# Optimization experiments

Measured on AMD Instinct MI355X. Metric: run time of the kernel, lower is better.

## Reference

```python
import jax, jax.numpy as jnp
import numpy as np

D_MODEL = 1024
N_HEADS = 16
HEAD_DIM = D_MODEL // N_HEADS
SCALE = HEAD_DIM ** -0.5
MIN_VAL = jnp.finfo(jnp.float32).min


def setup_inputs() -> dict:
    key = jax.random.key(0)
    ks = jax.random.split(key, 7)
    B, T = 1, 2048
    s = D_MODEL ** -0.5
    return {
        "x": jax.random.normal(ks[0], (B, T, D_MODEL), dtype=jnp.float32),
        "Wq": jax.random.normal(ks[1], (D_MODEL, D_MODEL), dtype=jnp.float32) * s,
        "Wk1": jax.random.normal(ks[2], (D_MODEL, D_MODEL), dtype=jnp.float32) * s,
        "Wk2": jax.random.normal(ks[3], (D_MODEL, D_MODEL), dtype=jnp.float32) * s,
        "Wv": jax.random.normal(ks[4], (D_MODEL, D_MODEL), dtype=jnp.float32) * s,
        "Wo": jax.random.normal(ks[5], (D_MODEL, D_MODEL), dtype=jnp.float32) * s,
        "lambda_logit": jnp.zeros((N_HEADS,), dtype=jnp.float32),  # logit(0.5)=0
    }


def _split_heads(y):
    B, T, _ = y.shape
    return y.reshape(B, T, N_HEADS, HEAD_DIM).transpose(0, 2, 1, 3)  # [B,H,T,hd]


def reference(x, Wq, Wk1, Wk2, Wv, Wo, lambda_logit):
    B, T, _ = x.shape
    q = _split_heads(x @ Wq.T)
    k1 = _split_heads(x @ Wk1.T)
    k2 = _split_heads(x @ Wk2.T)
    v = _split_heads(x @ Wv.T)

    s1 = jnp.einsum("bhqd,bhkd->bhqk", q, k1) * SCALE
    s2 = jnp.einsum("bhqd,bhkd->bhqk", q, k2) * SCALE

    causal = jnp.arange(T)[None, :] <= jnp.arange(T)[:, None]  # [T,T] keep mask
    s1 = jnp.where(causal[None, None], s1, MIN_VAL)
    s2 = jnp.where(causal[None, None], s2, MIN_VAL)

    attn_exp = jax.nn.softmax(s1, axis=-1)
    attn_noise = jax.nn.softmax(s2, axis=-1)
    lam = jax.nn.sigmoid(lambda_logit)[None, :, None, None]
    attn = attn_exp - lam * attn_noise
    denom = jnp.maximum(jnp.sum(jnp.abs(attn), axis=-1, keepdims=True), 1e-6)
    attn = attn / denom

    out = jnp.einsum("bhqk,bhkd->bhqd", attn, v)
    out = out.transpose(0, 2, 1, 3).reshape(B, T, D_MODEL)
    return out @ Wo.T
```

## Files before the change

kernel.cpp:

```cpp
#include <hip/hip_runtime.h>

#define T_SEQ 2048
#define DM 1024
#define NH 16
#define HD 64
#define SC2 0.1803368801111731f
#define LS 72

typedef unsigned short u16;
typedef unsigned int u32;
typedef __attribute__((ext_vector_type(8))) short bf16x8;
typedef __attribute__((ext_vector_type(4))) float f32x4;

static __device__ __forceinline__ f32x4 mfma16(bf16x8 a, bf16x8 b, f32x4 c) {
    return __builtin_amdgcn_mfma_f32_16x16x32_bf16(a, b, c, 0, 0, 0);
}
static __device__ __forceinline__ float bf2f(u16 u) {
    union { u32 i; float f; } v; v.i = ((u32)u) << 16; return v.f;
}
static __device__ __forceinline__ u16 f2bf(float f) {
    union { float f; u32 i; } v; v.f = f;
    u32 x = v.i;
    x += 0x7FFFu + ((x >> 16) & 1u);
    return (u16)(x >> 16);
}
static __device__ __forceinline__ u16 f2bf_t(float f) {
    union { float f; u32 i; } v; v.f = f;
    return (u16)(v.i >> 16);
}
static __device__ __forceinline__ u32 pk2(float lo, float hi) {
    return (u32)f2bf(lo) | ((u32)f2bf(hi) << 16);
}
static __device__ __forceinline__ float qsum16(float v) {
#pragma unroll
    for (int o = 1; o < 16; o <<= 1) v += __shfl_xor(v, o, 64);
    return v;
}
static __device__ __forceinline__ float ex2(float x) {
    return __builtin_amdgcn_exp2f(x);
}

static __device__ __forceinline__ void gl16(const u16* g, u16* l) {
    __builtin_amdgcn_global_load_lds(
        (const __attribute__((address_space(1))) void*)g,
        (__attribute__((address_space(3))) void*)l,
        16, 0, 0);
}

template <int NISS>
static __device__ __forceinline__ void stage_async(const u16* src, size_t row0,
                                                   size_t lds_, size_t col0,
                                                   u16* dst, int tid) {
#pragma unroll
    for (int it = 0; it < NISS; it++) {
        int r = it * 32 + (tid >> 3);
        int cg = (tid & 7) ^ (r & 7);
        gl16(&src[(row0 + r) * lds_ + col0 + cg * 8], &dst[(it * 256 + tid) * 8]);
    }
}
static __device__ __forceinline__ bf16x8 frag(const u16* buf, int R, int co) {
    return *(const bf16x8*)(&buf[R * 64 + co]);
}

__global__ __launch_bounds__(256) void detect_dtype(const u16* __restrict__ x,
                                                    int* __restrict__ flag) {
    __shared__ int tot;
    const int tid = threadIdx.x;
    if (tid == 0) tot = 0;
    __syncthreads();
    int c = 0;
#pragma unroll
    for (int i = 0; i < 4; i++) {
        u16 v = x[2 * (tid * 4 + i)];
        int e = (v >> 7) & 0xFF;
        c += (e >= 110 && e <= 140) ? 1 : 0;
    }
    atomicAdd(&tot, c);
    __syncthreads();
    if (tid == 0) *flag = (tot >= 512) ? 1 : 0;
}

__global__ __launch_bounds__(256) void cvt_bf16(
    const int* __restrict__ flag,
    const float* __restrict__ x, const float* __restrict__ wq,
    const float* __restrict__ wk1, const float* __restrict__ wk2,
    const float* __restrict__ wv, const float* __restrict__ wo,
    u16* __restrict__ xc, u16* __restrict__ wqc, u16* __restrict__ wk1c,
    u16* __restrict__ wk2c, u16* __restrict__ wvc, u16* __restrict__ woc) {
    if (*flag) return;
    const int b = blockIdx.x;
    const int tid = threadIdx.x;
    const float* src;
    u16* dst;
    int rel;
    if (b < 1024)      { src = x;   dst = xc;   rel = b; }
    else if (b < 1536) { src = wq;  dst = wqc;  rel = b - 1024; }
    else if (b < 2048) { src = wk1; dst = wk1c; rel = b - 1536; }
    else if (b < 2560) { src = wk2; dst = wk2c; rel = b - 2048; }
    else if (b < 3072) { src = wv;  dst = wvc;  rel = b - 2560; }
    else               { src = wo;  dst = woc;  rel = b - 3072; }
    size_t idx = (size_t)rel * 2048 + (size_t)tid * 8;
    const float* s = src + idx;
    uint4 a = *(const uint4*)s;
    uint4 bq = *(const uint4*)(s + 4);
    const float* af = (const float*)&a;
    const float* bf = (const float*)&bq;
    uint4 r;
    r.x = pk2(af[0], af[1]); r.y = pk2(af[2], af[3]);
    r.z = pk2(bf[0], bf[1]); r.w = pk2(bf[2], bf[3]);
    *(uint4*)(dst + idx) = r;
}

__global__ __launch_bounds__(256) void qkv_gemm(
    const int* __restrict__ flag,
    const void* __restrict__ x0, const void* __restrict__ wq0,
    const void* __restrict__ wk10, const void* __restrict__ wk20,
    const void* __restrict__ wv0,
    const u16* __restrict__ xc, const u16* __restrict__ wqc,
    const u16* __restrict__ wk1c, const u16* __restrict__ wk2c,
    const u16* __restrict__ wvc,
    u16* __restrict__ qd, u16* __restrict__ k1d, u16* __restrict__ k2d,
    u16* __restrict__ vtd) {
    __shared__ __align__(16) u16 As[2][128 * 64];
    __shared__ __align__(16) u16 Bs[2][128 * 64];

    const int f = *flag;
    const int tid = threadIdx.x;
    const int w = blockIdx.x >> 3;
    const int n0 = (blockIdx.x & 7) * 128;
    const int m0 = blockIdx.y * 128;
    const u16* xb = f ? (const u16*)x0 : xc;
    const u16* Bb;
    if (w == 0)      Bb = f ? (const u16*)wq0  : wqc;
    else if (w == 1) Bb = f ? (const u16*)wk10 : wk1c;
    else if (w == 2) Bb = f ? (const u16*)wk20 : wk2c;
    else             Bb = f ? (const u16*)wv0  : wvc;

    const int lane = tid & 63, wave = tid >> 6;
    const int lr = lane & 15, quad = lane >> 4;
    const int wm = (wave >> 1) * 64, wn = (wave & 1) * 64;
    const int sw = lr & 7;

    f32x4 acc[4][4];
#pragma unroll
    for (int i = 0; i < 4; i++)
#pragma unroll
        for (int j = 0; j < 4; j++) acc[i][j] = (f32x4){0.f, 0.f, 0.f, 0.f};

    stage_async<4>(xb, m0, DM, 0, As[0], tid);
    stage_async<4>(Bb, n0, DM, 0, Bs[0], tid);
    for (int k0 = 0; k0 < DM; k0 += 64) {
        const int cur = (k0 >> 6) & 1;
        __syncthreads();
        if (k0 + 64 < DM) {
            stage_async<4>(xb, m0, DM, k0 + 64, As[cur ^ 1], tid);
            stage_async<4>(Bb, n0, DM, k0 + 64, Bs[cur ^ 1], tid);
        }
#pragma unroll
        for (int kk = 0; kk < 2; kk++) {
            const int co = ((kk * 4 + quad) ^ sw) * 8;
            bf16x8 af[4], bfr[4];
#pragma unroll
            for (int i = 0; i < 4; i++) af[i] = frag(As[cur], wm + i * 16 + lr, co);
#pragma unroll
            for (int j = 0; j < 4; j++) bfr[j] = frag(Bs[cur], wn + j * 16 + lr, co);
#pragma unroll
            for (int i = 0; i < 4; i++)
#pragma unroll
                for (int j = 0; j < 4; j++) acc[i][j] = mfma16(af[i], bfr[j], acc[i][j]);
        }
    }

#pragma unroll
    for (int i = 0; i < 4; i++)
#pragma unroll
        for (int j = 0; j < 4; j++)
#pragma unroll
            for (int r = 0; r < 4; r++) {
                int t = m0 + wm + i * 16 + quad * 4 + r;
                int o = n0 + wn + j * 16 + lr;
                float val = acc[i][j][r];
                if (w == 0) val *= SC2;
                u16 vbits = f2bf(val);
                int hh = o >> 6, d0 = o & 63;
                if (w == 3)
                    vtd[((size_t)hh * HD + d0) * T_SEQ + t] = vbits;
                else
                    ((w == 0) ? qd : (w == 1) ? k1d : k2d)[((size_t)hh * T_SEQ + t) * HD + d0] = vbits;
            }
}

#define ATTN_MAP()                                            \
    const int b = blockIdx.x;                                 \
    const int par = b >> 9;                                   \
    const int rem = b & 511;                                  \
    const int h = rem & 15;                                   \
    const int bi = rem >> 4;                                  \
    const int qt = (bi < 16) ? bi : 47 - bi;                  \
    const int t0 = qt * 64;                                   \
    const int tid = threadIdx.x;                              \
    const int lane = tid & 63, wave = tid >> 6;               \
    const int lr = lane & 15, quad = lane >> 4;               \
    const int wm = wave * 16;                                 \
    const int sw = lr & 7;

__global__ __launch_bounds__(256) void attn_a(
    const u16* __restrict__ qg, const u16* __restrict__ k1g,
    const u16* __restrict__ k2g, float* __restrict__ zp) {
    __shared__ __align__(16) u16 k1s[64 * 64];
    __shared__ __align__(16) u16 k2s[64 * 64];
    ATTN_MAP();

    const u16* qh = qg + (size_t)h * T_SEQ * HD;
    const u16* k1h = k1g + (size_t)h * T_SEQ * HD;
    const u16* k2h = k2g + (size_t)h * T_SEQ * HD;

    bf16x8 aq[2];
#pragma unroll
    for (int kk = 0; kk < 2; kk++)
        aq[kk] = *(const bf16x8*)(&qh[(size_t)(t0 + wm + lr) * HD + kk * 32 + quad * 8]);

    float z1a[4] = {0.f, 0.f, 0.f, 0.f}, z2a[4] = {0.f, 0.f, 0.f, 0.f};

    for (int kt = par; kt <= qt; kt += 4) {
        __syncthreads();
        stage_async<2>(k1h, (size_t)kt * 64, HD, 0, k1s, tid);
        stage_async<2>(k2h, (size_t)kt * 64, HD, 0, k2s, tid);
        __syncthreads();

        f32x4 sa[4], sb[4];
#pragma unroll
        for (int j = 0; j < 4; j++) { sa[j] = (f32x4){0.f,0.f,0.f,0.f}; sb[j] = (f32x4){0.f,0.f,0.f,0.f}; }
#pragma unroll
        for (int kk = 0; kk < 2; kk++) {
            const int co = ((kk * 4 + quad) ^ sw) * 8;
#pragma unroll
            for (int j = 0; j < 4; j++) {
                sa[j] = mfma16(aq[kk], frag(k1s, j * 16 + lr, co), sa[j]);
                sb[j] = mfma16(aq[kk], frag(k2s, j * 16 + lr, co), sb[j]);
            }
        }

        if (kt < qt) {
#pragma unroll
            for (int r = 0; r < 4; r++)
#pragma unroll
                for (int j = 0; j < 4; j++) {
                    z1a[r] += ex2(sa[j][r]);
                    z2a[r] += ex2(sb[j][r]);
                }
        } else {
#pragma unroll
            for (int r = 0; r < 4; r++) {
                const int grow = t0 + wm + quad * 4 + r;
#pragma unroll
                for (int j = 0; j < 4; j++) {
                    int gcol = kt * 64 + j * 16 + lr;
                    if (gcol <= grow) {
                        z1a[r] += ex2(sa[j][r]);
                        z2a[r] += ex2(sb[j][r]);
                    }
                }
            }
        }
    }

#pragma unroll
    for (int r = 0; r < 4; r++) {
        float s1 = qsum16(z1a[r]);
        float s2 = qsum16(z2a[r]);
        if (lr == 0) {
            int row = t0 + wm + quad * 4 + r;
            zp[((size_t)(par * 2 + 0) * NH + h) * T_SEQ + row] = s1;
            zp[((size_t)(par * 2 + 1) * NH + h) * T_SEQ + row] = s2;
        }
    }
}

__global__ __launch_bounds__(256) void attn_b(
    const u16* __restrict__ qg, const u16* __restrict__ k1g,
    const u16* __restrict__ k2g, const u16* __restrict__ vtg,
    const float* __restrict__ zp, const void* __restrict__ lamsrc,
    const int* __restrict__ flag,
    float* __restrict__ dpart, u16* __restrict__ opart) {
    __shared__ __align__(16) u16 k1s[64 * 64];
    __shared__ __align__(16) u16 k2s[64 * 64];
    __shared__ __align__(16) u16 vs[64 * 64];
    __shared__ __align__(16) u16 ps[4][16 * LS];
    ATTN_MAP();

    const int f = *flag;
    float lamlogit = f ? bf2f(((const u16*)lamsrc)[h]) : ((const float*)lamsrc)[h];
    const float lam = 1.0f / (1.0f + __expf(-lamlogit));

    const u16* qh = qg + (size_t)h * T_SEQ * HD;
    const u16* k1h = k1g + (size_t)h * T_SEQ * HD;
    const u16* k2h = k2g + (size_t)h * T_SEQ * HD;
    const u16* vh = vtg + (size_t)h * HD * T_SEQ;

    bf16x8 aq[2];
#pragma unroll
    for (int kk = 0; kk < 2; kk++)
        aq[kk] = *(const bf16x8*)(&qh[(size_t)(t0 + wm + lr) * HD + kk * 32 + quad * 8]);

    float z1l[4], z2l[4];
#pragma unroll
    for (int r = 0; r < 4; r++) {
        int row = t0 + wm + quad * 4 + r;
        float z1 = 0.f, z2 = 0.f;
#pragma unroll
        for (int p = 0; p < 4; p++) {
            z1 += zp[((size_t)(p * 2 + 0) * NH + h) * T_SEQ + row];
            z2 += zp[((size_t)(p * 2 + 1) * NH + h) * T_SEQ + row];
        }
        z1l[r] = -__log2f(z1);
        z2l[r] = __log2f(lam) - __log2f(z2);
    }

    f32x4 oac[4];
#pragma unroll
    for (int j = 0; j < 4; j++) oac[j] = (f32x4){0.f, 0.f, 0.f, 0.f};
    float dacc[4] = {0.f, 0.f, 0.f, 0.f};

    for (int kt = par; kt <= qt; kt += 2) {
        __syncthreads();
        stage_async<2>(k1h, (size_t)kt * 64, HD, 0, k1s, tid);
        stage_async<2>(k2h, (size_t)kt * 64, HD, 0, k2s, tid);
        stage_async<2>(vh, 0, T_SEQ, (size_t)kt * 64, vs, tid);
        __syncthreads();

        f32x4 sa[4], sb[4];
#pragma unroll
        for (int j = 0; j < 4; j++) { sa[j] = (f32x4){0.f,0.f,0.f,0.f}; sb[j] = (f32x4){0.f,0.f,0.f,0.f}; }
#pragma unroll
        for (int kk = 0; kk < 2; kk++) {
            const int co = ((kk * 4 + quad) ^ sw) * 8;
#pragma unroll
            for (int j = 0; j < 4; j++) {
                sa[j] = mfma16(aq[kk], frag(k1s, j * 16 + lr, co), sa[j]);
                sb[j] = mfma16(aq[kk], frag(k2s, j * 16 + lr, co), sb[j]);
            }
        }

        if (kt < qt) {
#pragma unroll
            for (int r = 0; r < 4; r++)
#pragma unroll
                for (int j = 0; j < 4; j++) {
                    float p = ex2(sa[j][r] + z1l[r]) - ex2(sb[j][r] + z2l[r]);
                    dacc[r] += fabsf(p);
                    ps[wave][(quad * 4 + r) * LS + j * 16 + lr] = f2bf_t(p);
                }
        } else {
#pragma unroll
            for (int r = 0; r < 4; r++) {
                const int grow = t0 + wm + quad * 4 + r;
#pragma unroll
                for (int j = 0; j < 4; j++) {
                    int gcol = kt * 64 + j * 16 + lr;
                    float p = 0.f;
                    if (gcol <= grow)
                        p = ex2(sa[j][r] + z1l[r]) - ex2(sb[j][r] + z2l[r]);
                    dacc[r] += fabsf(p);
                    ps[wave][(quad * 4 + r) * LS + j * 16 + lr] = f2bf_t(p);
                }
            }
        }

#pragma unroll
        for (int kk = 0; kk < 2; kk++) {
            bf16x8 pa = *(const bf16x8*)(&ps[wave][lr * LS + kk * 32 + quad * 8]);
            const int co = ((kk * 4 + quad) ^ sw) * 8;
#pragma unroll
            for (int j = 0; j < 4; j++)
                oac[j] = mfma16(pa, frag(vs, j * 16 + lr, co), oac[j]);
        }
    }

#pragma unroll
    for (int r = 0; r < 4; r++) {
        float ds = qsum16(dacc[r]);
        if (lr == 0) {
            int row = t0 + wm + quad * 4 + r;
            dpart[((size_t)par * NH + h) * T_SEQ + row] = ds;
        }
    }
#pragma unroll
    for (int j = 0; j < 4; j++)
#pragma unroll
        for (int r = 0; r < 4; r++) {
            int row = t0 + wm + quad * 4 + r;
            opart[(size_t)par * T_SEQ * DM + (size_t)row * DM + h * HD + j * 16 + lr] =
                f2bf(oac[j][r]);
        }
}

__global__ __launch_bounds__(256) void normalize_o(
    const u16* __restrict__ opart, const float* __restrict__ dpart,
    u16* __restrict__ ao) {
    int g = blockIdx.x * 256 + threadIdx.x;
    int t = g >> 7;
    int cc = g & 127;
    int d0 = cc * 8;
    int h = d0 >> 6;
    float dsum = dpart[(size_t)h * T_SEQ + t] + dpart[(size_t)(NH + h) * T_SEQ + t];
    float rs = 1.f / fmaxf(dsum, 1e-6f);
    uint4 a = *(const uint4*)(&opart[(size_t)t * DM + d0]);
    uint4 bqq = *(const uint4*)(&opart[(size_t)T_SEQ * DM + (size_t)t * DM + d0]);
    const u32* au = (const u32*)&a;
    const u32* bu = (const u32*)&bqq;
    uint4 out;
    u32* ou = (u32*)&out;
#pragma unroll
    for (int i = 0; i < 4; i++) {
        float lo = (bf2f((u16)(au[i] & 0xFFFF)) + bf2f((u16)(bu[i] & 0xFFFF))) * rs;
        float hi = (bf2f((u16)(au[i] >> 16)) + bf2f((u16)(bu[i] >> 16))) * rs;
        ou[i] = pk2(lo, hi);
    }
    *(uint4*)(&ao[(size_t)t * DM + d0]) = out;
}

__global__ __launch_bounds__(256) void out_gemm(
    const u16* __restrict__ ab, const void* __restrict__ wo0,
    const u16* __restrict__ woc, const int* __restrict__ flag,
    void* __restrict__ outp) {
    __shared__ __align__(16) u16 As[2][64 * 64];
    __shared__ __align__(16) u16 Bs[2][64 * 64];

    const int f = *flag;
    const u16* wb = f ? (const u16*)wo0 : woc;
    const int n0 = blockIdx.x * 64;
    const int m0 = blockIdx.y * 64;
    const int tid = threadIdx.x;
    const int lane = tid & 63, wave = tid >> 6;
    const int lr = lane & 15, quad = lane >> 4;
    const int wm = (wave >> 1) * 32, wn = (wave & 1) * 32;
    const int sw = lr & 7;

    f32x4 acc[2][2];
#pragma unroll
    for (int i = 0; i < 2; i++)
#pragma unroll
        for (int j = 0; j < 2; j++) acc[i][j] = (f32x4){0.f, 0.f, 0.f, 0.f};

    stage_async<2>(ab, m0, DM, 0, As[0], tid);
    stage_async<2>(wb, n0, DM, 0, Bs[0], tid);
    for (int k0 = 0; k0 < DM; k0 += 64) {
        const int cur = (k0 >> 6) & 1;
        __syncthreads();
        if (k0 + 64 < DM) {
            stage_async<2>(ab, m0, DM, k0 + 64, As[cur ^ 1], tid);
            stage_async<2>(wb, n0, DM, k0 + 64, Bs[cur ^ 1], tid);
        }
#pragma unroll
        for (int kk = 0; kk < 2; kk++) {
            const int co = ((kk * 4 + quad) ^ sw) * 8;
            bf16x8 af[2], bfr[2];
#pragma unroll
            for (int i = 0; i < 2; i++) af[i] = frag(As[cur], wm + i * 16 + lr, co);
#pragma unroll
            for (int j = 0; j < 2; j++) bfr[j] = frag(Bs[cur], wn + j * 16 + lr, co);
#pragma unroll
            for (int i = 0; i < 2; i++)
#pragma unroll
                for (int j = 0; j < 2; j++) acc[i][j] = mfma16(af[i], bfr[j], acc[i][j]);
        }
    }

#pragma unroll
    for (int i = 0; i < 2; i++)
#pragma unroll
        for (int j = 0; j < 2; j++)
#pragma unroll
            for (int r = 0; r < 4; r++) {
                int t = m0 + wm + i * 16 + quad * 4 + r;
                int o = n0 + wn + j * 16 + lr;
                float val = acc[i][j][r];
                if (f)
                    ((u16*)outp)[(size_t)t * DM + o] = f2bf(val);
                else
                    ((float*)outp)[(size_t)t * DM + o] = val;
            }
}

extern "C" void kernel_launch(void* const* d_in, const int* in_sizes, int n_in,
                              void* d_out, int out_size, void* d_ws, size_t ws_size,
                              hipStream_t stream) {
    char* ws = (char*)d_ws;
    int* flag = (int*)(ws + 0);
    float* zp    = (float*)(ws + ((size_t)1 << 20));
    float* dpart = (float*)(ws + ((size_t)2 << 20));
    u16* qd  = (u16*)(ws + ((size_t)16 << 20));
    u16* k1d = (u16*)(ws + ((size_t)20 << 20));
    u16* k2d = (u16*)(ws + ((size_t)24 << 20));
    u16* vtd = (u16*)(ws + ((size_t)28 << 20));
    u16* ao  = (u16*)(ws + ((size_t)32 << 20));
    u16* opart = (u16*)(ws + ((size_t)36 << 20));
    u16* xc   = (u16*)(ws + ((size_t)44 << 20));
    u16* wqc  = (u16*)(ws + ((size_t)48 << 20));
    u16* wk1c = (u16*)(ws + ((size_t)50 << 20));
    u16* wk2c = (u16*)(ws + ((size_t)52 << 20));
    u16* wvc  = (u16*)(ws + ((size_t)54 << 20));
    u16* woc  = (u16*)(ws + ((size_t)56 << 20));

    detect_dtype<<<dim3(1), 256, 0, stream>>>((const u16*)d_in[0], flag);
    cvt_bf16<<<dim3(3584), 256, 0, stream>>>(
        flag, (const float*)d_in[0], (const float*)d_in[1], (const float*)d_in[2],
        (const float*)d_in[3], (const float*)d_in[4], (const float*)d_in[5],
        xc, wqc, wk1c, wk2c, wvc, woc);
    qkv_gemm<<<dim3(32, 16), 256, 0, stream>>>(
        flag, d_in[0], d_in[1], d_in[2], d_in[3], d_in[4],
        xc, wqc, wk1c, wk2c, wvc, qd, k1d, k2d, vtd);
    attn_a<<<dim3(2048), 256, 0, stream>>>(qd, k1d, k2d, zp);
    attn_b<<<dim3(1024), 256, 0, stream>>>(qd, k1d, k2d, vtd, zp, d_in[6], flag,
                                           dpart, opart);
    normalize_o<<<dim3(1024), 256, 0, stream>>>(opart, dpart, ao);
    out_gemm<<<dim3(16, 32), 256, 0, stream>>>(ao, d_in[5], woc, flag, d_out);
}
```

Baseline: 192.5 us.

## Process two 64-row query groups per attention block to reuse staged K/V tiles

Both attention kernels now handle a 128-row query tile per block, split into two 64-row groups that share each staged K1/K2/V tile in shared memory. This halves the block count and the global-to-LDS staging traffic per unit of work, which is meant to cut memory and synchronisation overhead. It costs more registers (doubled accumulators and Q fragments) and gives fewer blocks, which may reduce occupancy and load balance across CUs.

```diff
diff --git a/kernel.cpp b/kernel.cpp
--- a/kernel.cpp
+++ b/kernel.cpp
@@ -190,75 +190,86 @@
             }
 }
 
-#define ATTN_MAP()                                            \
-    const int b = blockIdx.x;                                 \
-    const int par = b >> 9;                                   \
-    const int rem = b & 511;                                  \
-    const int h = rem & 15;                                   \
-    const int bi = rem >> 4;                                  \
-    const int qt = (bi < 16) ? bi : 47 - bi;                  \
-    const int t0 = qt * 64;                                   \
-    const int tid = threadIdx.x;                              \
-    const int lane = tid & 63, wave = tid >> 6;               \
-    const int lr = lane & 15, quad = lane >> 4;               \
-    const int wm = wave * 16;                                 \
-    const int sw = lr & 7;
-
 __global__ __launch_bounds__(256) void attn_a(
     const u16* __restrict__ qg, const u16* __restrict__ k1g,
     const u16* __restrict__ k2g, float* __restrict__ zp) {
     __shared__ __align__(16) u16 k1s[64 * 64];
     __shared__ __align__(16) u16 k2s[64 * 64];
-    ATTN_MAP();
+    const int b = blockIdx.x;
+    const int par = b >> 8;
+    const int rem = b & 255;
+    const int h = rem & 15;
+    const int bi = rem >> 4;
+    const int qi = (bi < 8) ? bi : 23 - bi;
+    const int t0 = qi * 128;
+    const int tid = threadIdx.x;
+    const int lane = tid & 63, wave = tid >> 6;
+    const int lr = lane & 15, quad = lane >> 4;
+    const int wm = wave * 16;
+    const int sw = lr & 7;
 
     const u16* qh = qg + (size_t)h * T_SEQ * HD;
     const u16* k1h = k1g + (size_t)h * T_SEQ * HD;
     const u16* k2h = k2g + (size_t)h * T_SEQ * HD;
 
-    bf16x8 aq[2];
-#pragma unroll
-    for (int kk = 0; kk < 2; kk++)
-        aq[kk] = *(const bf16x8*)(&qh[(size_t)(t0 + wm + lr) * HD + kk * 32 + quad * 8]);
-
-    float z1a[4] = {0.f, 0.f, 0.f, 0.f}, z2a[4] = {0.f, 0.f, 0.f, 0.f};
-
-    for (int kt = par; kt <= qt; kt += 4) {
+    bf16x8 aq[2][2];
+#pragma unroll
+    for (int g = 0; g < 2; g++)
+#pragma unroll
+        for (int kk = 0; kk < 2; kk++)
+            aq[g][kk] = *(const bf16x8*)(
+                &qh[(size_t)(t0 + g * 64 + wm + lr) * HD + kk * 32 + quad * 8]);
+
+    float z1a[2][4], z2a[2][4];
+#pragma unroll
+    for (int g = 0; g < 2; g++)
+#pragma unroll
+        for (int r = 0; r < 4; r++) { z1a[g][r] = 0.f; z2a[g][r] = 0.f; }
+
+    const int ktmax = 2 * qi + 1;
+    for (int kt = par; kt <= ktmax; kt += 4) {
         __syncthreads();
         stage_async<2>(k1h, (size_t)kt * 64, HD, 0, k1s, tid);
         stage_async<2>(k2h, (size_t)kt * 64, HD, 0, k2s, tid);
         __syncthreads();
 
-        f32x4 sa[4], sb[4];
-#pragma unroll
-        for (int j = 0; j < 4; j++) { sa[j] = (f32x4){0.f,0.f,0.f,0.f}; sb[j] = (f32x4){0.f,0.f,0.f,0.f}; }
-#pragma unroll
-        for (int kk = 0; kk < 2; kk++) {
-            const int co = ((kk * 4 + quad) ^ sw) * 8;
-#pragma unroll
-            for (int j = 0; j < 4; j++) {
-                sa[j] = mfma16(aq[kk], frag(k1s, j * 16 + lr, co), sa[j]);
-                sb[j] = mfma16(aq[kk], frag(k2s, j * 16 + lr, co), sb[j]);
-            }
-        }
-
-        if (kt < qt) {
-#pragma unroll
-            for (int r = 0; r < 4; r++)
+#pragma unroll
+        for (int g = 0; g < 2; g++) {
+            const int row64 = 2 * qi + g;
+            if (kt > row64) continue;
+
+            f32x4 sa[4], sb[4];
+#pragma unroll
+            for (int j = 0; j < 4; j++) { sa[j] = (f32x4){0.f,0.f,0.f,0.f}; sb[j] = (f32x4){0.f,0.f,0.f,0.f}; }
+#pragma unroll
+            for (int kk = 0; kk < 2; kk++) {
+                const int co = ((kk * 4 + quad) ^ sw) * 8;
 #pragma unroll
                 for (int j = 0; j < 4; j++) {
-                    z1a[r] += ex2(sa[j][r]);
-                    z2a[r] += ex2(sb[j][r]);
+                    sa[j] = mfma16(aq[g][kk], frag(k1s, j * 16 + lr, co), sa[j]);
+                    sb[j] = mfma16(aq[g][kk], frag(k2s, j * 16 + lr, co), sb[j]);
                 }
-        } else {
-#pragma unroll
-            for (int r = 0; r < 4; r++) {
-                const int grow = t0 + wm + quad * 4 + r;
-#pragma unroll
-                for (int j = 0; j < 4; j++) {
-                    int gcol = kt * 64 + j * 16 + lr;
-                    if (gcol <= grow) {
-                        z1a[r] += ex2(sa[j][r]);
-                        z2a[r] += ex2(sb[j][r]);
+            }
+
+            if (kt < row64) {
+#pragma unroll
+                for (int r = 0; r < 4; r++)
+#pragma unroll
+                    for (int j = 0; j < 4; j++) {
+                        z1a[g][r] += ex2(sa[j][r]);
+                        z2a[g][r] += ex2(sb[j][r]);
+                    }
+            } else {
+#pragma unroll
+                for (int r = 0; r < 4; r++) {
+                    const int grow = t0 + g * 64 + wm + quad * 4 + r;
+#pragma unroll
+                    for (int j = 0; j < 4; j++) {
+                        int gcol = kt * 64 + j * 16 + lr;
+                        if (gcol <= grow) {
+                            z1a[g][r] += ex2(sa[j][r]);
+                            z2a[g][r] += ex2(sb[j][r]);
+                        }
                     }
                 }
             }
@@ -266,15 +277,17 @@
     }
 
 #pragma unroll
-    for (int r = 0; r < 4; r++) {
-        float s1 = qsum16(z1a[r]);
-        float s2 = qsum16(z2a[r]);
-        if (lr == 0) {
-            int row = t0 + wm + quad * 4 + r;
-            zp[((size_t)(par * 2 + 0) * NH + h) * T_SEQ + row] = s1;
-            zp[((size_t)(par * 2 + 1) * NH + h) * T_SEQ + row] = s2;
-        }
-    }
+    for (int g = 0; g < 2; g++)
+#pragma unroll
+        for (int r = 0; r < 4; r++) {
+            float s1 = qsum16(z1a[g][r]);
+            float s2 = qsum16(z2a[g][r]);
+            if (lr == 0) {
+                int row = t0 + g * 64 + wm + quad * 4 + r;
+                zp[((size_t)(par * 2 + 0) * NH + h) * T_SEQ + row] = s1;
+                zp[((size_t)(par * 2 + 1) * NH + h) * T_SEQ + row] = s2;
+            }
+        }
 }
 
 __global__ __launch_bounds__(256) void attn_b(
@@ -287,7 +300,18 @@
     __shared__ __align__(16) u16 k2s[64 * 64];
     __shared__ __align__(16) u16 vs[64 * 64];
     __shared__ __align__(16) u16 ps[4][16 * LS];
-    ATTN_MAP();
+    const int b = blockIdx.x;
+    const int par = b >> 8;
+    const int rem = b & 255;
+    const int h = rem & 15;
+    const int bi = rem >> 4;
+    const int qi = (bi < 8) ? bi : 23 - bi;
+    const int t0 = qi * 128;
+    const int tid = threadIdx.x;
+    const int lane = tid & 63, wave = tid >> 6;
+    const int lr = lane & 15, quad = lane >> 4;
+    const int wm = wave * 16;
+    const int sw = lr & 7;
 
     const int f = *flag;
     float lamlogit = f ? bf2f(((const u16*)lamsrc)[h]) : ((const float*)lamsrc)[h];
@@ -298,101 +322,123 @@
     const u16* k2h = k2g + (size_t)h * T_SEQ * HD;
     const u16* vh = vtg + (size_t)h * HD * T_SEQ;
 
-    bf16x8 aq[2];
-#pragma unroll
-    for (int kk = 0; kk < 2; kk++)
-        aq[kk] = *(const bf16x8*)(&qh[(size_t)(t0 + wm + lr) * HD + kk * 32 + quad * 8]);
-
-    float z1l[4], z2l[4];
-#pragma unroll
-    for (int r = 0; r < 4; r++) {
-        int row = t0 + wm + quad * 4 + r;
-        float z1 = 0.f, z2 = 0.f;
-#pragma unroll
-        for (int p = 0; p < 4; p++) {
-            z1 += zp[((size_t)(p * 2 + 0) * NH + h) * T_SEQ + row];
-            z2 += zp[((size_t)(p * 2 + 1) * NH + h) * T_SEQ + row];
-        }
-        z1l[r] = -__log2f(z1);
-        z2l[r] = __log2f(lam) - __log2f(z2);
-    }
-
-    f32x4 oac[4];
-#pragma unroll
-    for (int j = 0; j < 4; j++) oac[j] = (f32x4){0.f, 0.f, 0.f, 0.f};
-    float dacc[4] = {0.f, 0.f, 0.f, 0.f};
-
-    for (int kt = par; kt <= qt; kt += 2) {
+    bf16x8 aq[2][2];
+#pragma unroll
+    for (int g = 0; g < 2; g++)
+#pragma unroll
+        for (int kk = 0; kk < 2; kk++)
+            aq[g][kk] = *(const bf16x8*)(
+                &qh[(size_t)(t0 + g * 64 + wm + lr) * HD + kk * 32 + quad * 8]);
+
+    float z1l[2][4], z2l[2][4];
+#pragma unroll
+    for (int g = 0; g < 2; g++)
+#pragma unroll
+        for (int r = 0; r < 4; r++) {
+            int row = t0 + g * 64 + wm + quad * 4 + r;
+            float z1 = 0.f, z2 = 0.f;
+#pragma unroll
+            for (int p = 0; p < 4; p++) {
+                z1 += zp[((size_t)(p * 2 + 0) * NH + h) * T_SEQ + row];
+                z2 += zp[((size_t)(p * 2 + 1) * NH + h) * T_SEQ + row];
+            }
+            z1l[g][r] = -__log2f(z1);
+            z2l[g][r] = __log2f(lam) - __log2f(z2);
+        }
+
+    f32x4 oac[2][4];
+#pragma unroll
+    for (int g = 0; g < 2; g++)
+#pragma unroll
+        for (int j = 0; j < 4; j++) oac[g][j] = (f32x4){0.f, 0.f, 0.f, 0.f};
+    float dacc[2][4];
+#pragma unroll
+    for (int g = 0; g < 2; g++)
+#pragma unroll
+        for (int r = 0; r < 4; r++) dacc[g][r] = 0.f;
+
+    const int ktmax = 2 * qi + 1;
+    for (int kt = par; kt <= ktmax; kt += 2) {
         __syncthreads();
         stage_async<2>(k1h, (size_t)kt * 64, HD, 0, k1s, tid);
         stage_async<2>(k2h, (size_t)kt * 64, HD, 0, k2s, tid);
         stage_async<2>(vh, 0, T_SEQ, (size_t)kt * 64, vs, tid);
         __syncthreads();
 
-        f32x4 sa[4], sb[4];
-#pragma unroll
-        for (int j = 0; j < 4; j++) { sa[j] = (f32x4){0.f,0.f,0.f,0.f}; sb[j] = (f32x4){0.f,0.f,0.f,0.f}; }
-#pragma unroll
-        for (int kk = 0; kk < 2; kk++) {
-            const int co = ((kk * 4 + quad) ^ sw) * 8;
-#pragma unroll
-            for (int j = 0; j < 4; j++) {
-                sa[j] = mfma16(aq[kk], frag(k1s, j * 16 + lr, co), sa[j]);
-                sb[j] = mfma16(aq[kk], frag(k2s, j * 16 + lr, co), sb[j]);
-            }
-        }
-
-        if (kt < qt) {
-#pragma unroll
-            for (int r = 0; r < 4; r++)
+#pragma unroll
+        for (int g = 0; g < 2; g++) {
+            const int row64 = 2 * qi + g;
+            if (kt > row64) continue;
+
+            f32x4 sa[4], sb[4];
+#pragma unroll
+            for (int j = 0; j < 4; j++) { sa[j] = (f32x4){0.f,0.f,0.f,0.f}; sb[j] = (f32x4){0.f,0.f,0.f,0.f}; }
+#pragma unroll
+            for (int kk = 0; kk < 2; kk++) {
+                const int co = ((kk * 4 + quad) ^ sw) * 8;
 #pragma unroll
                 for (int j = 0; j < 4; j++) {
-                    float p = ex2(sa[j][r] + z1l[r]) - ex2(sb[j][r] + z2l[r]);
-                    dacc[r] += fabsf(p);
-                    ps[wave][(quad * 4 + r) * LS + j * 16 + lr] = f2bf_t(p);
+                    sa[j] = mfma16(aq[g][kk], frag(k1s, j * 16 + lr, co), sa[j]);
+                    sb[j] = mfma16(aq[g][kk], frag(k2s, j * 16 + lr, co), sb[j]);
                 }
-        } else {
+            }
+
+            if (kt < row64) {
+#pragma unroll
+                for (int r = 0; r < 4; r++)
+#pragma unroll
+                    for (int j = 0; j < 4; j++) {
+                        float p = ex2(sa[j][r] + z1l[g][r]) - ex2(sb[j][r] + z2l[g][r]);
+                        dacc[g][r] += fabsf(p);
+                        ps[wave][(quad * 4 + r) * LS + j * 16 + lr] = f2bf_t(p);
+                    }
+            } else {
+#pragma unroll
+                for (int r = 0; r < 4; r++) {
+                    const int grow = t0 + g * 64 + wm + quad * 4 + r;
+#pragma unroll
+                    for (int j = 0; j < 4; j++) {
+                        int gcol = kt * 64 + j * 16 + lr;
+                        float p = 0.f;
+                        if (gcol <= grow)
+                            p = ex2(sa[j][r] + z1l[g][r]) - ex2(sb[j][r] + z2l[g][r]);
+                        dacc[g][r] += fabsf(p);
+                        ps[wave][(quad * 4 + r) * LS + j * 16 + lr] = f2bf_t(p);
+                    }
+                }
+            }
+
+#pragma unroll
+            for (int kk = 0; kk < 2; kk++) {
+                bf16x8 pa = *(const bf16x8*)(&ps[wave][lr * LS + kk * 32 + quad * 8]);
+                const int co = ((kk * 4 + quad) ^ sw) * 8;
+#pragma unroll
+                for (int j = 0; j < 4; j++)
+                    oac[g][j] = mfma16(pa, frag(vs, j * 16 + lr, co), oac[g][j]);
+            }
+        }
+    }
+
+#pragma unroll
+    for (int g = 0; g < 2; g++)
+#pragma unroll
+        for (int r = 0; r < 4; r++) {
+            float ds = qsum16(dacc[g][r]);
+            if (lr == 0) {
+                int row = t0 + g * 64 + wm + quad * 4 + r;
+                dpart[((size_t)par * NH + h) * T_SEQ + row] = ds;
+            }
+        }
+#pragma unroll
+    for (int g = 0; g < 2; g++)
+#pragma unroll
+        for (int j = 0; j < 4; j++)
 #pragma unroll
             for (int r = 0; r < 4; r++) {
-                const int grow = t0 + wm + quad * 4 + r;
-#pragma unroll
-                for (int j = 0; j < 4; j++) {
-                    int gcol = kt * 64 + j * 16 + lr;
-                    float p = 0.f;
-                    if (gcol <= grow)
-                        p = ex2(sa[j][r] + z1l[r]) - ex2(sb[j][r] + z2l[r]);
-                    dacc[r] += fabsf(p);
-                    ps[wave][(quad * 4 + r) * LS + j * 16 + lr] = f2bf_t(p);
-                }
-            }
-        }
-
-#pragma unroll
-        for (int kk = 0; kk < 2; kk++) {
-            bf16x8 pa = *(const bf16x8*)(&ps[wave][lr * LS + kk * 32 + quad * 8]);
-            const int co = ((kk * 4 + quad) ^ sw) * 8;
-#pragma unroll
-            for (int j = 0; j < 4; j++)
-                oac[j] = mfma16(pa, frag(vs, j * 16 + lr, co), oac[j]);
-        }
-    }
-
-#pragma unroll
-    for (int r = 0; r < 4; r++) {
-        float ds = qsum16(dacc[r]);
-        if (lr == 0) {
-            int row = t0 + wm + quad * 4 + r;
-            dpart[((size_t)par * NH + h) * T_SEQ + row] = ds;
-        }
-    }
-#pragma unroll
-    for (int j = 0; j < 4; j++)
-#pragma unroll
-        for (int r = 0; r < 4; r++) {
-            int row = t0 + wm + quad * 4 + r;
-            opart[(size_t)par * T_SEQ * DM + (size_t)row * DM + h * HD + j * 16 + lr] =
-                f2bf(oac[j][r]);
-        }
+                int row = t0 + g * 64 + wm + quad * 4 + r;
+                opart[(size_t)par * T_SEQ * DM + (size_t)row * DM + h * HD + j * 16 + lr] =
+                    f2bf(oac[g][j][r]);
+            }
 }
 
 __global__ __launch_bounds__(256) void normalize_o(
@@ -511,9 +557,9 @@
     qkv_gemm<<<dim3(32, 16), 256, 0, stream>>>(
         flag, d_in[0], d_in[1], d_in[2], d_in[3], d_in[4],
         xc, wqc, wk1c, wk2c, wvc, qd, k1d, k2d, vtd);
-    attn_a<<<dim3(2048), 256, 0, stream>>>(qd, k1d, k2d, zp);
-    attn_b<<<dim3(1024), 256, 0, stream>>>(qd, k1d, k2d, vtd, zp, d_in[6], flag,
-                                           dpart, opart);
+    attn_a<<<dim3(1024), 256, 0, stream>>>(qd, k1d, k2d, zp);
+    attn_b<<<dim3(512), 256, 0, stream>>>(qd, k1d, k2d, vtd, zp, d_in[6], flag,
+                                          dpart, opart);
     normalize_o<<<dim3(1024), 256, 0, stream>>>(opart, dpart, ao);
     out_gemm<<<dim3(16, 32), 256, 0, stream>>>(ao, d_in[5], woc, flag, d_out);
 }
```

Measured after the change: 218.5 us. 13.5% more time.
